# Kernel optimization log

Hardware: AMD Instinct MI355X
Metric: run time of the kernel (lower is better)

## Reference

```python
import jax, jax.numpy as jnp
import numpy as np

B, NQ, QDIM = 4, 128, 512
EMB, HEADS = 512, 8
VOCAB, WDIM = 20000, 300
DH = EMB // HEADS
TAU = 1.0
LN_EPS = 1e-5


def setup_inputs() -> dict:
    key = jax.random.key(0)
    ks = jax.random.split(key, 8)
    s = lambda fan_in: 1.0 / np.sqrt(fan_in)
    return {
        "queries": jax.random.normal(ks[0], (B, NQ, QDIM), dtype=jnp.float32),
        "glove": jax.random.normal(ks[1], (VOCAB, WDIM), dtype=jnp.float32),
        # Linear weights stored as (in, out); y = x @ W (equivalent to torch x @ W.T)
        "Wq": jax.random.normal(ks[2], (QDIM, EMB), dtype=jnp.float32) * s(QDIM),
        "Wk": jax.random.normal(ks[3], (WDIM, EMB), dtype=jnp.float32) * s(WDIM),
        "Wv": jax.random.normal(ks[4], (WDIM, EMB), dtype=jnp.float32) * s(WDIM),
        "Wout": jax.random.normal(ks[5], (EMB, QDIM), dtype=jnp.float32) * s(EMB),
        "b_out": jnp.zeros((QDIM,), dtype=jnp.float32),
        "ln_g": jnp.ones((QDIM,), dtype=jnp.float32),
        "ln_b": jnp.zeros((QDIM,), dtype=jnp.float32),
    }


def _forward(queries, glove, Wq, Wk, Wv, Wout, b_out, ln_g, ln_b):
    b, nq, _ = queries.shape
    V = glove.shape[0]
    scale = DH ** -0.5

    # SubLayerConnection: x + sublayer(LayerNorm(x))
    mu = jnp.mean(queries, axis=-1, keepdims=True)
    var = jnp.mean(jnp.square(queries - mu), axis=-1, keepdims=True)
    xn = (queries - mu) * jax.lax.rsqrt(var + LN_EPS) * ln_g + ln_b

    # Projections. K/V of the GloVe table are batch-independent -> compute once.
    q = (xn @ Wq).reshape(b, nq, HEADS, DH)          # [b, nq, h, dh]
    k = (glove @ Wk).reshape(V, HEADS, DH)           # [V, h, dh]
    v = (glove @ Wv).reshape(V, HEADS, DH)           # [V, h, dh]

    # Attention scores over the whole vocabulary: [b, h, nq, V]
    dots = jnp.einsum("bqhd,vhd->bhqv", q, k) * scale

    # Gumbel-softmax, hard (straight-through)
    gkey = jax.random.key(42)
    u = jax.random.uniform(gkey, dots.shape, dtype=dots.dtype,
                           minval=jnp.finfo(dots.dtype).tiny, maxval=1.0)
    gumbels = (dots - jnp.log(-jnp.log(u))) / TAU
    y_soft = jax.nn.softmax(gumbels, axis=-1)
    idx = jnp.argmax(gumbels, axis=-1)               # argmax(softmax) == argmax(logits)
    y_hard = jax.nn.one_hot(idx, V, dtype=dots.dtype)
    attn = y_hard - jax.lax.stop_gradient(y_soft) + y_soft

    out = jnp.einsum("bhqv,vhd->bqhd", attn, v).reshape(b, nq, EMB)
    out = out @ Wout + b_out                          # dropout is identity in eval
    return queries + out


def reference(queries, glove, Wq, Wk, Wv, Wout, b_out, ln_g, ln_b):
    return _forward(queries, glove, Wq, Wk, Wv, Wout, b_out, ln_g, ln_b)
```

## Files before the change

### kernel.cpp

```cpp
#include <hip/hip_runtime.h>
#include <cstdint>
#include <cmath>

#define NB 4
#define NQn 128
#define QD 512
#define EMBD 512
#define NH 8
#define DHn 64
#define VOCAB 20000
#define WDn 300
#define VCHUNK 128
#define NCHUNK 157

typedef float f32x4 __attribute__((ext_vector_type(4)));
typedef float f32x2 __attribute__((ext_vector_type(2)));
typedef short bf16x8 __attribute__((ext_vector_type(8)));

__device__ __forceinline__ f32x2 lo2(f32x4 v) { return __builtin_shufflevector(v, v, 0, 1); }
__device__ __forceinline__ f32x2 hi2(f32x4 v) { return __builtin_shufflevector(v, v, 2, 3); }

__device__ __forceinline__ void pk_fma_blo(f32x2 &d, f32x2 a, f32x2 b) {
  asm("v_pk_fma_f32 %0, %1, %2, %0 op_sel:[0,0,0] op_sel_hi:[0,1,1]"
      : "+v"(d) : "v"(a), "v"(b));
}
__device__ __forceinline__ void pk_fma_bhi(f32x2 &d, f32x2 a, f32x2 b) {
  asm("v_pk_fma_f32 %0, %1, %2, %0 op_sel:[1,0,0] op_sel_hi:[1,1,1]"
      : "+v"(d) : "v"(a), "v"(b));
}

__device__ __forceinline__ uint32_t rotl(uint32_t x, int r) {
  return __builtin_amdgcn_alignbit(x, x, 32 - r);
}

__device__ __forceinline__ uint32_t cvt_pk_bf16(float a, float b) {
  uint32_t r;
  asm("v_cvt_pk_bf16_f32 %0, %1, %2" : "=v"(r) : "v"(a), "v"(b));
  return r;
}

__device__ __forceinline__ void split4(f32x4 v, uint2 &hi, uint2 &lo) {
  uint32_t h01 = cvt_pk_bf16(v.x, v.y);
  uint32_t h23 = cvt_pk_bf16(v.z, v.w);
  float rx = v.x - __uint_as_float(h01 << 16);
  float ry = v.y - __uint_as_float(h01 & 0xFFFF0000u);
  float rz = v.z - __uint_as_float(h23 << 16);
  float rw = v.w - __uint_as_float(h23 & 0xFFFF0000u);
  hi = make_uint2(h01, h23);
  lo = make_uint2(cvt_pk_bf16(rx, ry), cvt_pk_bf16(rz, rw));
}

#define TFK1 42u
#define TFK2 (0x1BD11BDAu ^ 42u)
__device__ __forceinline__ void tf8(uint32_t (&x0)[8], uint32_t (&x1)[8]) {
#define R8(r) \
  { _Pragma("unroll") for (int j = 0; j < 8; ++j) { x0[j] += x1[j]; x1[j] = rotl(x1[j], r); x1[j] ^= x0[j]; } }
#define K8(a, b) \
  { _Pragma("unroll") for (int j = 0; j < 8; ++j) { x0[j] += (a); x1[j] += (b); } }
  K8(0u, TFK1)
  R8(13) R8(15) R8(26) R8(6)  K8(TFK1, TFK2 + 1u)
  R8(17) R8(29) R8(16) R8(24) K8(TFK2, 0u + 2u)
  R8(13) R8(15) R8(26) R8(6)  K8(0u, TFK1 + 3u)
  R8(17) R8(29) R8(16) R8(24) K8(TFK1, TFK2 + 4u)
  R8(13) R8(15) R8(26) R8(6)  K8(TFK2, 0u + 5u)
#undef R8
#undef K8
}

__device__ __forceinline__ unsigned long long pack_key(float val, int idx) {
  uint32_t fb = __float_as_uint(val);
  uint32_t key = (fb & 0x80000000u) ? ~fb : (fb | 0x80000000u);
  return ((unsigned long long)key << 32) |
         (unsigned long long)(0xFFFFFFFFu - (uint32_t)idx);
}

#define BKk 60
__global__ __launch_bounds__(256, 4) void prep_kernel(
                             const float* __restrict__ queries,
                             const float* __restrict__ Wq,
                             const float* __restrict__ ln_g,
                             const float* __restrict__ ln_b,
                             const float* __restrict__ glove,
                             const float* __restrict__ Wk,
                             ushort* __restrict__ qh_ws,
                             ushort* __restrict__ ql_ws,
                             ushort* __restrict__ kh_ws,
                             ushort* __restrict__ kl_ws,
                             unsigned long long* __restrict__ pk_buf) {
  __shared__ __align__(16) char smem[31680];
  const int bid = blockIdx.x;
  const int tid = threadIdx.x;

  if (bid < 2560) {
    const int lo = bid & 7, h = (bid >> 3) & 7, vg = (bid >> 6) * 8 + lo;
    if (vg >= 313) return;
    const int v0 = vg * 64;
    const int n0 = h * 64;
    float (*AsT)[68] = (float(*)[68])smem;
    float (*Bs)[64]  = (float(*)[64])(smem + 16320);
    const int ty = tid >> 4, tx = tid & 15;
    f32x2 acc2[4][2] = {};
    for (int s = 0; s < 5; ++s) {
      const int w0 = s * BKk;
      __syncthreads();
      for (int f = tid; f < 64 * 15; f += 256) {
        int row = f / 15, c4 = f % 15;
        int v = v0 + row;
        float4 g4 = (v < VOCAB) ? *(const float4*)&glove[(size_t)v * WDn + w0 + c4 * 4]
                                : make_float4(0.f, 0.f, 0.f, 0.f);
        AsT[c4 * 4 + 0][row] = g4.x;
        AsT[c4 * 4 + 1][row] = g4.y;
        AsT[c4 * 4 + 2][row] = g4.z;
        AsT[c4 * 4 + 3][row] = g4.w;
      }
      for (int f = tid; f < BKk * 16; f += 256) {
        int row = f / 16, c4 = f % 16;
        *(float4*)&Bs[row][c4 * 4] = *(const float4*)&Wk[(size_t)(w0 + row) * EMBD + n0 + c4 * 4];
      }
      __syncthreads();
#pragma unroll 4
      for (int w = 0; w < BKk; ++w) {
        f32x4 aq = *(const f32x4*)&AsT[w][ty * 4];
        f32x4 bv = *(const f32x4*)&Bs[w][tx * 4];
        f32x2 bl = lo2(bv), bh = hi2(bv);
        f32x2 a01 = lo2(aq), a23 = hi2(aq);
        pk_fma_blo(acc2[0][0], a01, bl); pk_fma_blo(acc2[0][1], a01, bh);
        pk_fma_bhi(acc2[1][0], a01, bl); pk_fma_bhi(acc2[1][1], a01, bh);
        pk_fma_blo(acc2[2][0], a23, bl); pk_fma_blo(acc2[2][1], a23, bh);
        pk_fma_bhi(acc2[3][0], a23, bl); pk_fma_bhi(acc2[3][1], a23, bh);
      }
    }
#pragma unroll
    for (int i = 0; i < 4; ++i) {
      int v = v0 + ty * 4 + i;
      if (v < VOCAB) {
        f32x4 kv = {acc2[i][0].x, acc2[i][0].y, acc2[i][1].x, acc2[i][1].y};
        uint2 hi, lov;
        split4(kv, hi, lov);
        size_t off = ((size_t)h * VOCAB + v) * 64 + tx * 4;
        *(uint2*)&kh_ws[off] = hi;
        *(uint2*)&kl_ws[off] = lov;
      }
    }
  } else if (bid < 2816) {
    const int id = bid - 2560;
    const int bx = id & 127, by = id >> 7;
    float (*xnT)[4] = (float(*)[4])smem;
    const int wave = tid >> 6, lane = tid & 63;
    const int r0 = bx * 4;
    const int r = r0 + wave;

    float vals[8];
    float s = 0.f;
#pragma unroll
    for (int j = 0; j < 8; ++j) { vals[j] = queries[r * QD + j * 64 + lane]; s += vals[j]; }
#pragma unroll
    for (int m = 32; m >= 1; m >>= 1) s += __shfl_xor(s, m, 64);
    const float mu = s * (1.f / 512.f);
    float ss = 0.f;
#pragma unroll
    for (int j = 0; j < 8; ++j) { float d = vals[j] - mu; ss += d * d; }
#pragma unroll
    for (int m = 32; m >= 1; m >>= 1) ss += __shfl_xor(ss, m, 64);
    const float rstd = 1.f / sqrtf(ss * (1.f / 512.f) + 1e-5f);
#pragma unroll
    for (int j = 0; j < 8; ++j) {
      int e = j * 64 + lane;
      xnT[e][wave] = (vals[j] - mu) * rstd * ln_g[e] + ln_b[e];
    }
    __syncthreads();

    const int e = by * 256 + tid;
    float a0 = 0.f, a1 = 0.f, a2 = 0.f, a3 = 0.f;
#pragma unroll 4
    for (int i = 0; i < QD; ++i) {
      f32x4 xv = *(const f32x4*)&xnT[i][0];
      float w = Wq[i * EMBD + e];
      a0 += xv.x * w; a1 += xv.y * w; a2 += xv.z * w; a3 += xv.w * w;
    }
    const int h = e >> 6, d = e & 63;
    float aa[4] = {a0, a1, a2, a3};
#pragma unroll
    for (int i = 0; i < 4; ++i) {
      float q = aa[i] * 0.125f;
      uint32_t hp = cvt_pk_bf16(q, q);
      float resid = q - __uint_as_float(hp << 16);
      uint32_t lp = cvt_pk_bf16(resid, resid);
      size_t off = ((size_t)h * 512 + (r0 + i)) * 64 + d;
      qh_ws[off] = (ushort)(hp & 0xFFFFu);
      ql_ws[off] = (ushort)(lp & 0xFFFFu);
    }
  } else {
    for (int f = tid; f < NB * NH * NQn; f += 256) pk_buf[f] = 0ull;
  }
}

template<bool FULL>
__device__ __forceinline__ void score_epi(const f32x4 (&acc)[8],
                                          int v0, int tx, int ty, int rowtile, int h,
                                          unsigned long long* __restrict__ pk_buf) {
#pragma unroll
  for (int i = 0; i < 4; ++i) {
    const int r = rowtile * 128 + ty * 4 + i;
    const int b = r >> 7, q = r & 127;
    const int rowidx = (b * NH + h) * NQn + q;
    const uint32_t base = (uint32_t)rowidx * (uint32_t)VOCAB;

    uint32_t x0[8], x1[8];
#pragma unroll
    for (int j = 0; j < 8; ++j) {
      x0[j] = 0u;
      x1[j] = base + (uint32_t)(v0 + tx + 16 * j);
    }
    tf8(x0, x1);

    float best = -INFINITY; int bidx = 0x7fffffff;
#pragma unroll
    for (int j = 0; j < 8; ++j) {
      int v = v0 + tx + 16 * j;
      if (FULL || v < VOCAB) {
        uint32_t bits = x0[j] ^ x1[j];
        float f = __uint_as_float((bits >> 9) | 0x3f800000u) - 1.0f;
        float u = fmaxf(f, 1.17549435e-38f);
        float t = __log2f(u);
        float s = __log2f(-t);
        float val = fmaf(-0.69314718f, s, acc[j][i]);
        if (val > best) { best = val; bidx = v; }
      }
    }
#pragma unroll
    for (int m = 8; m >= 1; m >>= 1) {
      float ov = __shfl_xor(best, m, 64);
      int   oi = __shfl_xor(bidx, m, 64);
      if (ov > best || (ov == best && oi < bidx)) { best = ov; bidx = oi; }
    }
    if (tx == 0) atomicMax(&pk_buf[rowidx], pack_key(best, bidx));
  }
}

__global__ __launch_bounds__(512, 8) void score_kernel(
                  const ushort* __restrict__ qh_ws,
                  const ushort* __restrict__ ql_ws,
                  const ushort* __restrict__ kh_ws,
                  const ushort* __restrict__ kl_ws,
                  unsigned long long* __restrict__ pk_buf) {
  __shared__ uint4 lds4[2048];
  char* const Kh = (char*)lds4;
  char* const Kl = Kh + 16384;
  const int tid = threadIdx.x;
  const int id = blockIdx.x;
  const int h = id & 7, rowtile = (id >> 3) & 3, chunk = id >> 5;
  const int v0 = chunk * VCHUNK;
  const int tx = tid & 15, ty = tid >> 4;
  const int w = tid >> 6;
  const int g4 = (tid >> 4) & 3;
  const int swz = (tx & 7) << 4;

  for (int f = tid; f < 128 * 8; f += 512) {
    int row = f >> 3, c8 = f & 7;
    int v = v0 + row;
    uint4 vh = {0u, 0u, 0u, 0u}, vl = {0u, 0u, 0u, 0u};
    if (v < VOCAB) {
      size_t off = ((size_t)h * VOCAB + v) * 64 + c8 * 8;
      vh = *(const uint4*)(kh_ws + off);
      vl = *(const uint4*)(kl_ws + off);
    }
    int loff = (row * 128 + c8 * 16) ^ ((row & 7) << 4);
    *(uint4*)(Kh + loff) = vh;
    *(uint4*)(Kl + loff) = vl;
  }

  bf16x8 aH[2], aL[2];
  {
    const size_t qbase = ((size_t)h * 512 + rowtile * 128 + w * 16 + tx) * 64 + g4 * 8;
#pragma unroll
    for (int kh = 0; kh < 2; ++kh) {
      aH[kh] = *(const bf16x8*)(qh_ws + qbase + kh * 32);
      aL[kh] = *(const bf16x8*)(ql_ws + qbase + kh * 32);
    }
  }
  __syncthreads();

  f32x4 acc[8] = {};
#pragma unroll
  for (int ct = 0; ct < 8; ++ct) {
    const int bbase = (ct * 16 + tx) * 128 + g4 * 16;
    bf16x8 bH[2], bL[2];
#pragma unroll
    for (int kh = 0; kh < 2; ++kh) {
      int off = (bbase + kh * 64) ^ swz;
      bH[kh] = *(const bf16x8*)(Kh + off);
      bL[kh] = *(const bf16x8*)(Kl + off);
    }
    acc[ct] = __builtin_amdgcn_mfma_f32_16x16x32_bf16(aH[0], bH[0], acc[ct], 0, 0, 0);
    acc[ct] = __builtin_amdgcn_mfma_f32_16x16x32_bf16(aH[1], bH[1], acc[ct], 0, 0, 0);
    acc[ct] = __builtin_amdgcn_mfma_f32_16x16x32_bf16(aH[0], bL[0], acc[ct], 0, 0, 0);
    acc[ct] = __builtin_amdgcn_mfma_f32_16x16x32_bf16(aH[1], bL[1], acc[ct], 0, 0, 0);
    acc[ct] = __builtin_amdgcn_mfma_f32_16x16x32_bf16(aL[0], bH[0], acc[ct], 0, 0, 0);
    acc[ct] = __builtin_amdgcn_mfma_f32_16x16x32_bf16(aL[1], bH[1], acc[ct], 0, 0, 0);
    acc[ct] = __builtin_amdgcn_mfma_f32_16x16x32_bf16(aL[0], bL[0], acc[ct], 0, 0, 0);
    acc[ct] = __builtin_amdgcn_mfma_f32_16x16x32_bf16(aL[1], bL[1], acc[ct], 0, 0, 0);
  }

  if (v0 + VCHUNK <= VOCAB)
    score_epi<true>(acc, v0, tx, ty, rowtile, h, pk_buf);
  else
    score_epi<false>(acc, v0, tx, ty, rowtile, h, pk_buf);
}

__global__ __launch_bounds__(512, 8) void out_kernel(
                           const float* __restrict__ queries,
                           const float* __restrict__ glove,
                           const float* __restrict__ Wv,
                           const float* __restrict__ Wout,
                           const float* __restrict__ b_out,
                           const unsigned long long* __restrict__ pk_buf,
                           float* __restrict__ out) {
  __shared__ float gl[NH][WDn];
  __shared__ float vrow[EMBD];
  __shared__ int idxs[NH];
  const int tid = threadIdx.x;
  const int r = blockIdx.x, b = r >> 7, q = r & 127;
  if (tid < NH) {
    unsigned long long p = pk_buf[(b * NH + tid) * NQn + q];
    idxs[tid] = (int)(0xFFFFFFFFu - (uint32_t)(p & 0xFFFFFFFFull));
  }
  __syncthreads();
  for (int f = tid; f < NH * 75; f += 512) {
    int hh = f / 75, c4 = f % 75;
    *(float4*)&gl[hh][c4 * 4] = *(const float4*)&glove[(size_t)idxs[hh] * WDn + c4 * 4];
  }
  __syncthreads();
  {
    const int e = tid, hh = e >> 6;
    float a = 0.f;
    for (int w = 0; w < WDn; ++w) a += gl[hh][w] * Wv[(size_t)w * EMBD + e];
    vrow[e] = a;
  }
  __syncthreads();
  {
    const int j = tid;
    float o = 0.f;
    for (int e = 0; e < EMBD; ++e) o += vrow[e] * Wout[(size_t)e * QD + j];
    out[(size_t)r * QD + j] = queries[(size_t)r * QD + j] + o + b_out[j];
  }
}

extern "C" void kernel_launch(void* const* d_in, const int* in_sizes, int n_in,
                              void* d_out, int out_size, void* d_ws, size_t ws_size,
                              hipStream_t stream) {
  const float* queries = (const float*)d_in[0];
  const float* glove   = (const float*)d_in[1];
  const float* Wq      = (const float*)d_in[2];
  const float* Wk      = (const float*)d_in[3];
  const float* Wv      = (const float*)d_in[4];
  const float* Wout    = (const float*)d_in[5];
  const float* b_out   = (const float*)d_in[6];
  const float* ln_g    = (const float*)d_in[7];
  const float* ln_b    = (const float*)d_in[8];
  float* out = (float*)d_out;

  char* ws = (char*)d_ws;
  ushort* qh_ws = (ushort*)ws;
  ushort* ql_ws = qh_ws + (size_t)NH * 512 * 64;
  ushort* kh_ws = ql_ws + (size_t)NH * 512 * 64;
  ushort* kl_ws = kh_ws + (size_t)NH * VOCAB * 64;
  unsigned long long* pk_buf = (unsigned long long*)(kl_ws + (size_t)NH * VOCAB * 64);

  hipLaunchKernelGGL(prep_kernel, dim3(2817), dim3(256), 0, stream,
                     queries, Wq, ln_g, ln_b, glove, Wk,
                     qh_ws, ql_ws, kh_ws, kl_ws, pk_buf);
  hipLaunchKernelGGL(score_kernel, dim3(5024), dim3(512), 0, stream,
                     qh_ws, ql_ws, kh_ws, kl_ws, pk_buf);
  hipLaunchKernelGGL(out_kernel, dim3(512), dim3(512), 0, stream,
                     queries, glove, Wv, Wout, b_out, pk_buf, out);
}
```

Measured before the change: 316.8 us.

## Compute glove K projection with split-bf16 MFMA instead of packed FP32 FMA

Rewrites the glove×Wk projection in the prep kernel to split each fp32 operand into bf16 hi/lo parts and accumulate four MFMA 16x16x32 products per k-slice. Tiles are stored in XOR-swizzled LDS to avoid bank conflicts. This targets the FP32 vector-ALU cost of the large vocabulary projection. The cost is extra conversion work during tile loads, scalar 16-bit output stores, and a small precision change from the bf16x3-style approximation.

```diff
diff --git a/kernel.cpp b/kernel.cpp
--- a/kernel.cpp
+++ b/kernel.cpp
@@ -14,20 +14,7 @@
 #define NCHUNK 157
 
 typedef float f32x4 __attribute__((ext_vector_type(4)));
-typedef float f32x2 __attribute__((ext_vector_type(2)));
 typedef short bf16x8 __attribute__((ext_vector_type(8)));
-
-__device__ __forceinline__ f32x2 lo2(f32x4 v) { return __builtin_shufflevector(v, v, 0, 1); }
-__device__ __forceinline__ f32x2 hi2(f32x4 v) { return __builtin_shufflevector(v, v, 2, 3); }
-
-__device__ __forceinline__ void pk_fma_blo(f32x2 &d, f32x2 a, f32x2 b) {
-  asm("v_pk_fma_f32 %0, %1, %2, %0 op_sel:[0,0,0] op_sel_hi:[0,1,1]"
-      : "+v"(d) : "v"(a), "v"(b));
-}
-__device__ __forceinline__ void pk_fma_bhi(f32x2 &d, f32x2 a, f32x2 b) {
-  asm("v_pk_fma_f32 %0, %1, %2, %0 op_sel:[1,0,0] op_sel_hi:[1,1,1]"
-      : "+v"(d) : "v"(a), "v"(b));
-}
 
 __device__ __forceinline__ uint32_t rotl(uint32_t x, int r) {
   return __builtin_amdgcn_alignbit(x, x, 32 - r);
@@ -74,7 +61,6 @@
          (unsigned long long)(0xFFFFFFFFu - (uint32_t)idx);
 }
 
-#define BKk 60
 __global__ __launch_bounds__(256, 4) void prep_kernel(
                              const float* __restrict__ queries,
                              const float* __restrict__ Wq,
@@ -87,7 +73,7 @@
                              ushort* __restrict__ kh_ws,
                              ushort* __restrict__ kl_ws,
                              unsigned long long* __restrict__ pk_buf) {
-  __shared__ __align__(16) char smem[31680];
+  __shared__ __align__(16) char smem[32768];
   const int bid = blockIdx.x;
   const int tid = threadIdx.x;
 
@@ -96,50 +82,95 @@
     if (vg >= 313) return;
     const int v0 = vg * 64;
     const int n0 = h * 64;
-    float (*AsT)[68] = (float(*)[68])smem;
-    float (*Bs)[64]  = (float(*)[64])(smem + 16320);
-    const int ty = tid >> 4, tx = tid & 15;
-    f32x2 acc2[4][2] = {};
+    char* const Gh = smem;
+    char* const Gl = smem + 8192;
+    char* const Wh = smem + 16384;
+    char* const Wl = smem + 24576;
+    const int w = tid >> 6, lane = tid & 63;
+    const int txl = lane & 15;
+    const int g4 = (lane >> 4) & 3;
+    const int swzA = (txl & 7) << 4;
+
+    f32x4 acc[4] = {};
+
     for (int s = 0; s < 5; ++s) {
-      const int w0 = s * BKk;
+      const int k0 = s * 64;
       __syncthreads();
-      for (int f = tid; f < 64 * 15; f += 256) {
-        int row = f / 15, c4 = f % 15;
-        int v = v0 + row;
-        float4 g4 = (v < VOCAB) ? *(const float4*)&glove[(size_t)v * WDn + w0 + c4 * 4]
-                                : make_float4(0.f, 0.f, 0.f, 0.f);
-        AsT[c4 * 4 + 0][row] = g4.x;
-        AsT[c4 * 4 + 1][row] = g4.y;
-        AsT[c4 * 4 + 2][row] = g4.z;
-        AsT[c4 * 4 + 3][row] = g4.w;
-      }
-      for (int f = tid; f < BKk * 16; f += 256) {
-        int row = f / 16, c4 = f % 16;
-        *(float4*)&Bs[row][c4 * 4] = *(const float4*)&Wk[(size_t)(w0 + row) * EMBD + n0 + c4 * 4];
+      for (int f = tid; f < 64 * 16; f += 256) {
+        int row = f >> 4, c4 = f & 15;
+        int v = v0 + row, kk = k0 + c4 * 4;
+        f32x4 g = {0.f, 0.f, 0.f, 0.f};
+        if (v < VOCAB && kk + 4 <= WDn)
+          g = *(const f32x4*)&glove[(size_t)v * WDn + kk];
+        uint2 hi, lov;
+        split4(g, hi, lov);
+        int off = (row * 128 + c4 * 8) ^ ((row & 7) << 4);
+        *(uint2*)(Gh + off) = hi;
+        *(uint2*)(Gl + off) = lov;
+      }
+      for (int f = tid; f < 64 * 16; f += 256) {
+        int kk = f >> 4, d4 = f & 15;
+        int kg = k0 + kk;
+        f32x4 wv = {0.f, 0.f, 0.f, 0.f};
+        if (kg < WDn)
+          wv = *(const f32x4*)&Wk[(size_t)kg * EMBD + n0 + d4 * 4];
+        uint2 hi, lov;
+        split4(wv, hi, lov);
+        ushort hs[4] = {(ushort)(hi.x & 0xFFFFu), (ushort)(hi.x >> 16),
+                        (ushort)(hi.y & 0xFFFFu), (ushort)(hi.y >> 16)};
+        ushort ls[4] = {(ushort)(lov.x & 0xFFFFu), (ushort)(lov.x >> 16),
+                        (ushort)(lov.y & 0xFFFFu), (ushort)(lov.y >> 16)};
+#pragma unroll
+        for (int j = 0; j < 4; ++j) {
+          int d = d4 * 4 + j;
+          int off = (d * 128 + kk * 2) ^ ((d & 7) << 4);
+          *(ushort*)(Wh + off) = hs[j];
+          *(ushort*)(Wl + off) = ls[j];
+        }
       }
       __syncthreads();
-#pragma unroll 4
-      for (int w = 0; w < BKk; ++w) {
-        f32x4 aq = *(const f32x4*)&AsT[w][ty * 4];
-        f32x4 bv = *(const f32x4*)&Bs[w][tx * 4];
-        f32x2 bl = lo2(bv), bh = hi2(bv);
-        f32x2 a01 = lo2(aq), a23 = hi2(aq);
-        pk_fma_blo(acc2[0][0], a01, bl); pk_fma_blo(acc2[0][1], a01, bh);
-        pk_fma_bhi(acc2[1][0], a01, bl); pk_fma_bhi(acc2[1][1], a01, bh);
-        pk_fma_blo(acc2[2][0], a23, bl); pk_fma_blo(acc2[2][1], a23, bh);
-        pk_fma_bhi(acc2[3][0], a23, bl); pk_fma_bhi(acc2[3][1], a23, bh);
-      }
-    }
-#pragma unroll
-    for (int i = 0; i < 4; ++i) {
-      int v = v0 + ty * 4 + i;
-      if (v < VOCAB) {
-        f32x4 kv = {acc2[i][0].x, acc2[i][0].y, acc2[i][1].x, acc2[i][1].y};
-        uint2 hi, lov;
-        split4(kv, hi, lov);
-        size_t off = ((size_t)h * VOCAB + v) * 64 + tx * 4;
-        *(uint2*)&kh_ws[off] = hi;
-        *(uint2*)&kl_ws[off] = lov;
+
+      bf16x8 aH[2], aL[2];
+#pragma unroll
+      for (int kh = 0; kh < 2; ++kh) {
+        int off = ((w * 16 + txl) * 128 + (g4 * 8 + kh * 32) * 2) ^ swzA;
+        aH[kh] = *(const bf16x8*)(Gh + off);
+        aL[kh] = *(const bf16x8*)(Gl + off);
+      }
+#pragma unroll
+      for (int ct = 0; ct < 4; ++ct) {
+        bf16x8 bH[2], bL[2];
+#pragma unroll
+        for (int kh = 0; kh < 2; ++kh) {
+          int off = ((ct * 16 + txl) * 128 + (g4 * 8 + kh * 32) * 2) ^ swzA;
+          bH[kh] = *(const bf16x8*)(Wh + off);
+          bL[kh] = *(const bf16x8*)(Wl + off);
+        }
+        acc[ct] = __builtin_amdgcn_mfma_f32_16x16x32_bf16(aH[0], bH[0], acc[ct], 0, 0, 0);
+        acc[ct] = __builtin_amdgcn_mfma_f32_16x16x32_bf16(aH[1], bH[1], acc[ct], 0, 0, 0);
+        acc[ct] = __builtin_amdgcn_mfma_f32_16x16x32_bf16(aH[0], bL[0], acc[ct], 0, 0, 0);
+        acc[ct] = __builtin_amdgcn_mfma_f32_16x16x32_bf16(aH[1], bL[1], acc[ct], 0, 0, 0);
+        acc[ct] = __builtin_amdgcn_mfma_f32_16x16x32_bf16(aL[0], bH[0], acc[ct], 0, 0, 0);
+        acc[ct] = __builtin_amdgcn_mfma_f32_16x16x32_bf16(aL[1], bH[1], acc[ct], 0, 0, 0);
+        acc[ct] = __builtin_amdgcn_mfma_f32_16x16x32_bf16(aL[0], bL[0], acc[ct], 0, 0, 0);
+        acc[ct] = __builtin_amdgcn_mfma_f32_16x16x32_bf16(aL[1], bL[1], acc[ct], 0, 0, 0);
+      }
+    }
+
+#pragma unroll
+    for (int ct = 0; ct < 4; ++ct) {
+#pragma unroll
+      for (int i = 0; i < 4; ++i) {
+        int v = v0 + w * 16 + (lane >> 4) * 4 + i;
+        if (v < VOCAB) {
+          float x = acc[ct][i];
+          uint32_t hp = cvt_pk_bf16(x, x);
+          float resid = x - __uint_as_float(hp << 16);
+          uint32_t lp = cvt_pk_bf16(resid, resid);
+          size_t off = ((size_t)h * VOCAB + v) * 64 + ct * 16 + txl;
+          kh_ws[off] = (ushort)(hp & 0xFFFFu);
+          kl_ws[off] = (ushort)(lp & 0xFFFFu);
+        }
       }
     }
   } else if (bid < 2816) {
```

After: 304.6 us. 3.8% less time.
